# Optimization experiments

Measured on AMD Instinct MI355X. Metric: run time of the kernel, lower is better.

The kernel has to match this reference:

```python
import jax, jax.numpy as jnp
import numpy as np

DIM = 256  # channel width
B, H, W = 4, 64, 64


def conv2d(x, w, b, pad, groups=1):
    # x: NCHW, w: OIHW (I = C_in/groups)
    y = jax.lax.conv_general_dilated(
        x, w, window_strides=(1, 1),
        padding=[(pad[0], pad[0]), (pad[1], pad[1])],
        dimension_numbers=("NCHW", "OIHW", "NCHW"),
        feature_group_count=groups)
    return y + b[None, :, None, None]


def l2norm(x, eps=1e-12):
    # matches F.normalize(x, dim=-1): x / max(||x||_2, eps)
    n = jnp.sqrt(jnp.sum(x * x, axis=-1, keepdims=True))
    return x / jnp.maximum(n, eps)


def setup_inputs() -> dict:
    key = jax.random.key(0)
    ks = jax.random.split(key, 12)
    dim, c8 = DIM, DIM // 8
    w = lambda k, shape, s: jax.random.normal(k, shape, jnp.float32) * s
    return {
        "x": jax.random.normal(ks[0], (B, dim, H, W), jnp.float32),
        "w_conv": w(ks[1], (dim, dim, 3, 3), 0.02), "b_conv": jnp.zeros((dim,), jnp.float32),
        "w01": w(ks[2], (dim, 1, 1, 7), 0.05), "b01": jnp.zeros((dim,), jnp.float32),
        "w02": w(ks[3], (dim, 1, 7, 1), 0.05), "b02": jnp.zeros((dim,), jnp.float32),
        "w11": w(ks[4], (dim, 1, 1, 11), 0.05), "b11": jnp.zeros((dim,), jnp.float32),
        "w12": w(ks[5], (dim, 1, 11, 1), 0.05), "b12": jnp.zeros((dim,), jnp.float32),
        "w21": w(ks[6], (dim, 1, 1, 21), 0.05), "b21": jnp.zeros((dim,), jnp.float32),
        "w22": w(ks[7], (dim, 1, 21, 1), 0.05), "b22": jnp.zeros((dim,), jnp.float32),
        "w_proj": w(ks[8], (c8, dim, 1, 1), 0.05), "b_proj": jnp.zeros((c8,), jnp.float32),
        "w3": w(ks[9], (c8, dim // 4, 1, 1), 0.05), "b3": jnp.zeros((c8,), jnp.float32),
        "w4": w(ks[10], (dim, c8, 1, 1), 0.05), "b4": jnp.zeros((dim,), jnp.float32),
    }


def reference(x, w_conv, b_conv, w01, b01, w02, b02, w11, b11, w12, b12,
              w21, b21, w22, b22, w_proj, b_proj, w3, b3, w4, b4):
    b, c, h, w_ = x.shape
    x = conv2d(x, w_conv, b_conv, (1, 1))
    # multi-scale separable depthwise convs (7, 11, 21)
    x1 = conv2d(conv2d(x, w01, b01, (0, 3), c), w02, b02, (3, 0), c)
    x2 = conv2d(conv2d(x, w11, b11, (0, 5), c), w12, b12, (5, 0), c)
    x3 = conv2d(conv2d(x, w21, b21, (0, 10), c), w22, b22, (10, 0), c)
    out1 = x1 + x2 + x3 + x                      # [b, dim, h, w]
    out1 = conv2d(out1, w_proj, b_proj, (0, 0))  # [b, dim//8, h, w]
    c8 = out1.shape[1]
    t = out1.reshape(b, c8, h * w_)              # b head c (h w), head=1

    q1 = l2norm(t)
    attn1 = jax.nn.softmax(q1 @ jnp.swapaxes(q1, -2, -1), axis=-1)  # [b, c8, c8]
    out2 = attn1 @ t                                                # [b, c8, hw]

    # branch 2: spatial attention (hw x hw)
    ts = jnp.swapaxes(t, -2, -1)                 # [b, hw, c8]
    q2 = l2norm(ts)
    attn2 = jax.nn.softmax(q2 @ jnp.swapaxes(q2, -2, -1), axis=-1)  # [b, hw, hw]
    out3 = jnp.swapaxes(attn2 @ ts, -2, -1)                         # [b, c8, hw]

    out4 = jnp.concatenate([out2.reshape(b, c8, h, w_),
                            out3.reshape(b, c8, h, w_)], axis=1)    # [b, dim//4, h, w]
    out5 = conv2d(out4, w3, b3, (0, 0)) + out1
    return conv2d(out5, w4, b4, (0, 0))          # [b, dim, h, w]
```

## Files before the change

### kernel.cpp

```cpp
#include <hip/hip_runtime.h>
#include <hip/hip_bf16.h>

typedef __hip_bfloat16 bf16;
typedef short s16;
typedef __attribute__((ext_vector_type(4))) short s16x4;
typedef __attribute__((ext_vector_type(8))) short s16x8;
typedef __attribute__((ext_vector_type(4))) float f32x4;

__device__ __forceinline__ s16 f2b(float f){
    unsigned u = __float_as_uint(f);
    unsigned r = (u + 0x7FFFu + ((u >> 16) & 1u)) >> 16;
    return (s16)r;
}
__device__ __forceinline__ float b2f_bits(s16 v){
    return __uint_as_float(((unsigned)(unsigned short)v) << 16);
}

__global__ __launch_bounds__(256) void xtrans_k(const float* __restrict__ x, s16* __restrict__ xcl){
    __shared__ s16 lb[64][258];
    int h = blockIdx.x, b = blockIdx.y, t = threadIdx.x;
    for (int i = t; i < 16384; i += 256){
        int ci = i >> 6, w = i & 63;
        lb[w][ci] = f2b(x[((b*256 + ci)*64 + h)*64 + w]);
    }
    __syncthreads();
    for (int i = t; i < 16384; i += 256){
        int w = i >> 8, ci = i & 255;
        xcl[(b*4096 + h*64 + w)*256 + ci] = lb[w][ci];
    }
}

__global__ __launch_bounds__(256) void wpack_k(const float* __restrict__ w, s16* __restrict__ wpk){
    int idx = blockIdx.x*256 + threadIdx.x;
    int cil = idx & 31;
    int r   = idx >> 5;
    int co  = r & 255;
    int r2  = r >> 8;
    int tap = r2 % 9, cc = r2 / 9;
    wpk[idx] = f2b(w[(co*256 + cc*32 + cil)*9 + tap]);
}

__global__ __launch_bounds__(256) void conv3x3m_k(const s16* __restrict__ xcl,
        const s16* __restrict__ wpk, const float* __restrict__ bias,
        bf16* __restrict__ y0){
    __shared__ alignas(16) s16 smem[30240];
    s16* xls = smem;
    s16* wls = smem + 9504;
    const int sp = blockIdx.x, cog = blockIdx.y;
    const int b = sp >> 5, h0 = (sp & 31)*2;
    const int t = threadIdx.x;
    const int wv = t >> 6, lane = t & 63;
    const int lm = lane & 15, g = lane >> 4;

    f32x4 acc[2][4];
    #pragma unroll
    for (int mi = 0; mi < 2; ++mi)
        #pragma unroll
        for (int ni = 0; ni < 4; ++ni) acc[mi][ni] = (f32x4){0.f,0.f,0.f,0.f};

    for (int cc = 0; cc < 8; ++cc){
        __syncthreads();
        for (int i = t; i < 1056; i += 256){
            int g8 = i & 3, wi = (i>>2) % 66, r = (i>>2) / 66;
            int h = h0 - 1 + r, w = wi - 1;
            s16x8 v = {0,0,0,0,0,0,0,0};
            if (h >= 0 && h < 64 && w >= 0 && w < 64)
                v = *(const s16x8*)&xcl[(b*4096 + h*64 + w)*256 + cc*32 + g8*8];
            s16* d = &xls[(r*66 + wi)*36 + g8*8];
            *(s16x4*)d       = __builtin_shufflevector(v, v, 0,1,2,3);
            *(s16x4*)(d + 4) = __builtin_shufflevector(v, v, 4,5,6,7);
        }
        for (int i = t; i < 2304; i += 256){
            int g8 = i & 3, co = (i>>2) & 63, tap = i >> 8;
            s16x8 v = *(const s16x8*)&wpk[((cc*9 + tap)*256 + cog*64 + co)*32 + g8*8];
            s16* d = &wls[(tap*64 + co)*36 + g8*8];
            *(s16x4*)d       = __builtin_shufflevector(v, v, 0,1,2,3);
            *(s16x4*)(d + 4) = __builtin_shufflevector(v, v, 4,5,6,7);
        }
        __syncthreads();
        #pragma unroll
        for (int tap = 0; tap < 9; ++tap){
            const int kh = tap/3, kw = tap%3;
            s16x8 bfr[4], afr[2];
            #pragma unroll
            for (int ni = 0; ni < 4; ++ni){
                const s16* p = &wls[(tap*64 + ni*16 + lm)*36 + g*8];
                s16x4 lo = *(const s16x4*)p;
                s16x4 hi = *(const s16x4*)(p + 4);
                bfr[ni] = __builtin_shufflevector(lo, hi, 0,1,2,3,4,5,6,7);
            }
            #pragma unroll
            for (int mi = 0; mi < 2; ++mi){
                int m = (wv*2 + mi)*16 + lm;
                int hr = m >> 6, ww = m & 63;
                const s16* p = &xls[((hr + kh)*66 + (ww + kw))*36 + g*8];
                s16x4 lo = *(const s16x4*)p;
                s16x4 hi = *(const s16x4*)(p + 4);
                afr[mi] = __builtin_shufflevector(lo, hi, 0,1,2,3,4,5,6,7);
            }
            #pragma unroll
            for (int mi = 0; mi < 2; ++mi)
                #pragma unroll
                for (int ni = 0; ni < 4; ++ni)
                    acc[mi][ni] = __builtin_amdgcn_mfma_f32_16x16x32_bf16(
                        afr[mi], bfr[ni], acc[mi][ni], 0, 0, 0);
        }
    }
    __syncthreads();
    float* ot = (float*)smem;
    #pragma unroll
    for (int mi = 0; mi < 2; ++mi)
        #pragma unroll
        for (int ni = 0; ni < 4; ++ni)
            #pragma unroll
            for (int r = 0; r < 4; ++r){
                int m  = (wv*2 + mi)*16 + g*4 + r;
                int co = ni*16 + lm;
                ot[co*132 + m] = acc[mi][ni][r];
            }
    __syncthreads();
    for (int i = t; i < 8192; i += 256){
        int co = i >> 7, m = i & 127;
        float v = ot[co*132 + m] + bias[cog*64 + co];
        y0[((b*256 + cog*64 + co)*64 + h0 + (m>>6))*64 + (m & 63)] = __float2bfloat16(v);
    }
}

template<int K>
__device__ __forceinline__ void sep_branch(const float (*__restrict__ pl)[65], float (*__restrict__ hp)[65],
                                           int c, int t,
                                           const float* __restrict__ wh, const float* __restrict__ bh,
                                           const float* __restrict__ wv, const float* __restrict__ bv,
                                           float* acc){
    constexpr int P = K/2;
    constexpr int W = 16 + 2*P;
    float wk[K];
    #pragma unroll
    for (int j = 0; j < K; ++j) wk[j] = wh[c*K + j];
    float bhv = bh[c];
    {
        int h = t >> 2, w0 = (t & 3)*16;
        float win[W];
        #pragma unroll
        for (int j = 0; j < W; ++j){
            int ww = w0 - P + j;
            win[j] = (ww >= 0 && ww < 64) ? pl[h][ww] : 0.f;
        }
        __syncthreads();
        #pragma unroll
        for (int i = 0; i < 16; ++i){
            float s = bhv;
            #pragma unroll
            for (int k = 0; k < K; ++k) s += win[i+k]*wk[k];
            hp[h][w0 + i] = s;
        }
    }
    float vk[K];
    #pragma unroll
    for (int j = 0; j < K; ++j) vk[j] = wv[c*K + j];
    float bvv = bv[c];
    __syncthreads();
    {
        int w = t & 63, h0 = (t >> 6)*16;
        float win[W];
        #pragma unroll
        for (int j = 0; j < W; ++j){
            int hh = h0 - P + j;
            win[j] = (hh >= 0 && hh < 64) ? hp[hh][w] : 0.f;
        }
        #pragma unroll
        for (int i = 0; i < 16; ++i){
            float s = bvv;
            #pragma unroll
            for (int k = 0; k < K; ++k) s += win[i+k]*vk[k];
            acc[i] += s;
        }
    }
}

__global__ __launch_bounds__(256) void sepconv_k(const bf16* __restrict__ y0,
        const float* __restrict__ w01, const float* __restrict__ b01,
        const float* __restrict__ w02, const float* __restrict__ b02,
        const float* __restrict__ w11, const float* __restrict__ b11,
        const float* __restrict__ w12, const float* __restrict__ b12,
        const float* __restrict__ w21, const float* __restrict__ b21,
        const float* __restrict__ w22, const float* __restrict__ b22,
        bf16* __restrict__ out1){
    __shared__ float pl[64][65];
    __shared__ float hp[64][65];
    int bc = blockIdx.x;
    int c = bc & 255;
    int t = threadIdx.x;
    const bf16* src = y0 + bc*4096;
    for (int i = t; i < 4096; i += 256) pl[i>>6][i&63] = __bfloat162float(src[i]);
    __syncthreads();
    float acc[16];
    #pragma unroll
    for (int k = 0; k < 16; ++k) acc[k] = 0.f;
    sep_branch<7 >(pl, hp, c, t, w01, b01, w02, b02, acc);
    sep_branch<11>(pl, hp, c, t, w11, b11, w12, b12, acc);
    sep_branch<21>(pl, hp, c, t, w21, b21, w22, b22, acc);
    bf16* dst = out1 + bc*4096;
    {
        int w = t & 63, h0 = (t >> 6)*16;
        #pragma unroll
        for (int i = 0; i < 16; ++i)
            dst[(h0 + i)*64 + w] = __float2bfloat16(acc[i] + pl[h0 + i][w]);
    }
}

__global__ __launch_bounds__(256) void proj_k(const bf16* __restrict__ out1, const float* __restrict__ wp,
                                              const float* __restrict__ bp, float* __restrict__ tbuf,
                                              s16* __restrict__ tTb, float* __restrict__ rn2){
    __shared__ float wl[256*32];
    __shared__ s16 part[4][64][36];
    int pt = blockIdx.x, b = blockIdx.y, t = threadIdx.x;
    int q = t >> 6, lane = t & 63;
    for (int i = t; i < 8192; i += 256){
        int ci = i >> 5, cc = i & 31;
        wl[ci*32 + cc] = wp[cc*256 + ci];
    }
    __syncthreads();
    int p = pt*64 + lane;
    float acc[32] = {};
    const bf16* xb = out1 + b*1048576 + p;
    for (int ci = q*64; ci < q*64 + 64; ++ci){
        float v = __bfloat162float(xb[ci*4096]);
        const float* wr = &wl[ci*32];
        #pragma unroll
        for (int c8 = 0; c8 < 8; ++c8){
            float4 w4 = *(const float4*)&wr[c8*4];
            acc[c8*4+0] += w4.x*v; acc[c8*4+1] += w4.y*v;
            acc[c8*4+2] += w4.z*v; acc[c8*4+3] += w4.w*v;
        }
    }
    #pragma unroll
    for (int cc = 0; cc < 32; ++cc) part[q][lane][cc] = f2b(acc[cc]);
    __syncthreads();
    int p_loc = t >> 2, qq = t & 3;
    int pg = pt*64 + p_loc;
    float a8[8];
    float ss = 0.f;
    #pragma unroll
    for (int c = 0; c < 8; ++c){
        int cc = qq*8 + c;
        float v = b2f_bits(part[0][p_loc][cc]) + b2f_bits(part[1][p_loc][cc])
                + b2f_bits(part[2][p_loc][cc]) + b2f_bits(part[3][p_loc][cc]) + bp[cc];
        a8[c] = v;
        ss += v*v;
    }
    ss += __shfl_xor(ss, 1, 4);
    ss += __shfl_xor(ss, 2, 4);
    if (qq == 0) rn2[b*4096 + pg] = 1.f / fmaxf(sqrtf(ss), 1e-12f);
    #pragma unroll
    for (int c = 0; c < 8; ++c) tbuf[(b*32 + qq*8 + c)*4096 + pg] = a8[c];
    s16x8 o8;
    #pragma unroll
    for (int c = 0; c < 8; ++c) o8[c] = f2b(a8[c]);
    *(s16x8*)&tTb[(b*4096 + pg)*32 + qq*8] = o8;
}

__global__ __launch_bounds__(256) void gram2_k(const float* __restrict__ tbuf, float* __restrict__ part){
    __shared__ float tl[128][33];
    int ps = blockIdx.x, b = blockIdx.y, t = threadIdx.x;
    for (int idx = t; idx < 4096; idx += 256){
        int cc = idx >> 7, pp = idx & 127;
        tl[pp][cc] = tbuf[(b*32+cc)*4096 + ps*128 + pp];
    }
    __syncthreads();
    #pragma unroll
    for (int k = 0; k < 4; ++k){
        int pair = k*256 + t;
        int i = pair >> 5, j = pair & 31;
        float s = 0.f;
        #pragma unroll 4
        for (int pp = 0; pp < 128; ++pp) s += tl[pp][i]*tl[pp][j];
        part[(b*32+ps)*1024 + pair] = s;
    }
}

__global__ __launch_bounds__(64) void attn1_k(const float* __restrict__ part,
                                              float* __restrict__ attn1T){
    int i = blockIdx.x, b = blockIdx.y, j = threadIdx.x;
    float gij = 0.f, gjj = 0.f;
    if (j < 32){
        #pragma unroll 8
        for (int ps = 0; ps < 32; ++ps){
            const float* pp = part + (b*32+ps)*1024;
            gij += pp[i*32 + j];
            gjj += pp[j*33];
        }
    }
    float rnj = 1.f / fmaxf(sqrtf(gjj), 1e-12f);
    float rni = __shfl(rnj, i, 64);
    float e = (j < 32) ? __expf(rni*rnj*gij) : 0.f;
    float sum = e;
    #pragma unroll
    for (int o = 32; o > 0; o >>= 1) sum += __shfl_xor(sum, o, 64);
    if (j < 32) attn1T[b*1024 + j*32 + i] = e / sum;
}

__global__ __launch_bounds__(256) void fold_k(const float* __restrict__ attn1T,
        const float* __restrict__ w3, const float* __restrict__ b3,
        const float* __restrict__ w4, const float* __restrict__ b4,
        float* __restrict__ WtT, float* __restrict__ WoT, float* __restrict__ bfo){
    __shared__ float a1[1024];
    __shared__ float w3a[1024];
    __shared__ float w3bs[1024];
    int b = blockIdx.x, t = threadIdx.x;
    for (int idx = t; idx < 1024; idx += 256){
        int i = idx >> 5, j = idx & 31;
        a1[idx]   = attn1T[b*1024 + j*32 + i];
        w3bs[idx] = w3[i*64 + 32 + j];
    }
    __syncthreads();
    for (int idx = t; idx < 1024; idx += 256){
        int cc = idx >> 5, j = idx & 31;
        float s = 0.f;
        #pragma unroll 8
        for (int i = 0; i < 32; ++i) s += w3[cc*64 + i]*a1[i*32 + j];
        w3a[idx] = s;
    }
    __syncthreads();
    int co = t;
    float w4r[32];
    #pragma unroll
    for (int cc = 0; cc < 32; ++cc) w4r[cc] = w4[co*32 + cc];
    float bfv = b4[co];
    #pragma unroll
    for (int cc = 0; cc < 32; ++cc) bfv += w4r[cc]*b3[cc];
    bfo[b*256 + co] = bfv;
    for (int j = 0; j < 32; ++j){
        float st = w4r[j];
        float so = 0.f;
        #pragma unroll 8
        for (int cc = 0; cc < 32; ++cc){
            st += w4r[cc]*w3a[cc*32 + j];
            so += w4r[cc]*w3bs[cc*32 + j];
        }
        WtT[(b*32 + j)*256 + co] = st;
        WoT[(b*32 + j)*256 + co] = so;
    }
}

__global__ __launch_bounds__(256) void flashm_k(const s16* __restrict__ tTb, const float* __restrict__ rn2,
                                                float* __restrict__ partA, float* __restrict__ partL){
    __shared__ alignas(16) s16 kvb[128*36];
    __shared__ alignas(16) s16 vts[32*132];
    __shared__ alignas(16) s16 pls[4][16*132];
    __shared__ float rnj[128];
    __shared__ float ri[64];
    const int ib = blockIdx.x, b = blockIdx.y, chunk = blockIdx.z;
    const int t = threadIdx.x, wv = t >> 6, lane = t & 63;
    const int lm = lane & 15, g = lane >> 4;
    const int i0 = ib*64;

    if (t < 64) ri[t] = rn2[b*4096 + i0 + t];
    s16x8 qf = *(const s16x8*)&tTb[(b*4096 + i0 + wv*16 + lm)*32 + g*8];
    __syncthreads();
    float rni4[4];
    #pragma unroll
    for (int r = 0; r < 4; ++r) rni4[r] = ri[wv*16 + g*4 + r];

    f32x4 oacc[2];
    oacc[0] = (f32x4){0.f,0.f,0.f,0.f};
    oacc[1] = (f32x4){0.f,0.f,0.f,0.f};
    float lacc[4] = {0.f,0.f,0.f,0.f};
    s16* pw = pls[wv];

    for (int jt = chunk*16; jt < chunk*16 + 16; ++jt){
        const int j0 = jt*128;
        __syncthreads();
        for (int gi = t; gi < 512; gi += 256){
            int j = gi >> 2, g8 = gi & 3;
            s16x8 v = *(const s16x8*)&tTb[(b*4096 + j0 + j)*32 + g8*8];
            s16* d = &kvb[j*36 + g8*8];
            *(s16x4*)d       = __builtin_shufflevector(v, v, 0,1,2,3);
            *(s16x4*)(d + 4) = __builtin_shufflevector(v, v, 4,5,6,7);
            #pragma unroll
            for (int e = 0; e < 8; ++e) vts[(g8*8 + e)*132 + j] = v[e];
        }
        if (t < 128) rnj[t] = rn2[b*4096 + j0 + t];
        __syncthreads();
        #pragma unroll
        for (int nt = 0; nt < 8; ++nt){
            const s16* bp = &kvb[(nt*16 + lm)*36 + g*8];
            s16x4 blo = *(const s16x4*)bp;
            s16x4 bhi = *(const s16x4*)(bp + 4);
            s16x8 bf = __builtin_shufflevector(blo, bhi, 0,1,2,3,4,5,6,7);
            f32x4 s = __builtin_amdgcn_mfma_f32_16x16x32_bf16(qf, bf,
                        (f32x4){0.f,0.f,0.f,0.f}, 0, 0, 0);
            float rj = rnj[nt*16 + lm];
            #pragma unroll
            for (int r = 0; r < 4; ++r){
                float e = __expf(s[r]*rni4[r]*rj);
                lacc[r] += e;
                pw[(g*4 + r)*132 + nt*16 + lm] = f2b(e);
            }
        }
        #pragma unroll
        for (int ks = 0; ks < 4; ++ks){
            const s16* ap = &pw[lm*132 + ks*32 + g*8];
            s16x4 alo = *(const s16x4*)ap;
            s16x4 ahi = *(const s16x4*)(ap + 4);
            s16x8 af = __builtin_shufflevector(alo, ahi, 0,1,2,3,4,5,6,7);
            #pragma unroll
            for (int n2 = 0; n2 < 2; ++n2){
                const s16* vp = &vts[(n2*16 + lm)*132 + ks*32 + g*8];
                s16x4 vlo = *(const s16x4*)vp;
                s16x4 vhi = *(const s16x4*)(vp + 4);
                s16x8 vf = __builtin_shufflevector(vlo, vhi, 0,1,2,3,4,5,6,7);
                oacc[n2] = __builtin_amdgcn_mfma_f32_16x16x32_bf16(af, vf, oacc[n2], 0, 0, 0);
            }
        }
    }
    #pragma unroll
    for (int r = 0; r < 4; ++r){
        float v = lacc[r];
        v += __shfl_xor(v, 1, 16); v += __shfl_xor(v, 2, 16);
        v += __shfl_xor(v, 4, 16); v += __shfl_xor(v, 8, 16);
        lacc[r] = v;
    }
    const int base = (b*2 + chunk)*4096 + i0 + wv*16;
    #pragma unroll
    for (int n2 = 0; n2 < 2; ++n2)
        #pragma unroll
        for (int r = 0; r < 4; ++r)
            partA[(base + g*4 + r)*32 + n2*16 + lm] = oacc[n2][r];
    if (lm == 0){
        #pragma unroll
        for (int r = 0; r < 4; ++r) partL[base + g*4 + r] = lacc[r];
    }
}

__global__ __launch_bounds__(256) void finalfuse_k(const float* __restrict__ tbuf,
        const float* __restrict__ partA, const float* __restrict__ partL,
        const float* __restrict__ WtT, const float* __restrict__ WoT,
        const float* __restrict__ bfo, float* __restrict__ out){
    int pt = blockIdx.x, cog = blockIdx.y, b = blockIdx.z, t = threadIdx.x;
    int p = pt*256 + t;
    float l = partL[(b*2 + 0)*4096 + p] + partL[(b*2 + 1)*4096 + p];
    float inv = 1.f / l;
    const float* pa0 = partA + ((b*2 + 0)*4096 + p)*32;
    const float* pa1 = partA + ((b*2 + 1)*4096 + p)*32;
    float v3[32];
    #pragma unroll
    for (int q = 0; q < 8; ++q){
        float4 a = *(const float4*)&pa0[q*4];
        float4 c = *(const float4*)&pa1[q*4];
        v3[q*4+0] = (a.x + c.x)*inv; v3[q*4+1] = (a.y + c.y)*inv;
        v3[q*4+2] = (a.z + c.z)*inv; v3[q*4+3] = (a.w + c.w)*inv;
    }
    float acc[32];
    #pragma unroll
    for (int co = 0; co < 32; ++co) acc[co] = bfo[b*256 + cog*32 + co];
    for (int j = 0; j < 32; ++j){
        float vt = tbuf[(b*32 + j)*4096 + p];
        float vo = v3[j];
        const float* wtr = WtT + (b*32 + j)*256 + cog*32;
        const float* wor = WoT + (b*32 + j)*256 + cog*32;
        #pragma unroll
        for (int co = 0; co < 32; ++co) acc[co] += wtr[co]*vt + wor[co]*vo;
    }
    #pragma unroll
    for (int co = 0; co < 32; ++co)
        out[((b*256 + cog*32 + co)*4096) + p] = acc[co];
}

extern "C" void kernel_launch(void* const* d_in, const int* in_sizes, int n_in,
                              void* d_out, int out_size, void* d_ws, size_t ws_size,
                              hipStream_t stream) {
    const float* x      = (const float*)d_in[0];
    const float* w_conv = (const float*)d_in[1];
    const float* b_conv = (const float*)d_in[2];
    const float* w01 = (const float*)d_in[3];  const float* b01 = (const float*)d_in[4];
    const float* w02 = (const float*)d_in[5];  const float* b02 = (const float*)d_in[6];
    const float* w11 = (const float*)d_in[7];  const float* b11 = (const float*)d_in[8];
    const float* w12 = (const float*)d_in[9];  const float* b12 = (const float*)d_in[10];
    const float* w21 = (const float*)d_in[11]; const float* b21 = (const float*)d_in[12];
    const float* w22 = (const float*)d_in[13]; const float* b22 = (const float*)d_in[14];
    const float* w_proj = (const float*)d_in[15]; const float* b_proj = (const float*)d_in[16];
    const float* w3 = (const float*)d_in[17]; const float* b3 = (const float*)d_in[18];
    const float* w4 = (const float*)d_in[19]; const float* b4 = (const float*)d_in[20];

    char* wsb = (char*)d_ws;
    s16*   xcl  = (s16*)wsb;
    bf16*  out1 = (bf16*)wsb;
    bf16*  y0   = (bf16*)(wsb + 8388608);
    s16*   wpk  = (s16*)(wsb + 16777216);
    float* f    = (float*)d_ws;
    float* part   = f + 0;
    float* partA  = f + 0;
    float* tbuf   = f + 2097152;
    s16*   tTb    = (s16*)(wsb + 10485760);
    float* WtT    = f + 3145728;
    float* WoT    = f + 3178496;
    float* bfo    = f + 3211264;
    float* partL  = f + 4194304;
    float* attn1T = f + 4722816;
    float* rn2    = f + 4726912;

    xtrans_k<<<dim3(64, 4), 256, 0, stream>>>(x, xcl);
    wpack_k<<<dim3(2304), 256, 0, stream>>>(w_conv, wpk);
    conv3x3m_k<<<dim3(128, 4), 256, 0, stream>>>(xcl, wpk, b_conv, y0);
    sepconv_k<<<dim3(1024), 256, 0, stream>>>(y0, w01, b01, w02, b02,
                                              w11, b11, w12, b12,
                                              w21, b21, w22, b22, out1);
    proj_k<<<dim3(64, 4), 256, 0, stream>>>(out1, w_proj, b_proj, tbuf, tTb, rn2);
    gram2_k<<<dim3(32, 4), 256, 0, stream>>>(tbuf, part);
    attn1_k<<<dim3(32, 4), 64, 0, stream>>>(part, attn1T);
    fold_k<<<dim3(4), 256, 0, stream>>>(attn1T, w3, b3, w4, b4, WtT, WoT, bfo);
    flashm_k<<<dim3(64, 4, 2), 256, 0, stream>>>(tTb, rn2, partA, partL);
    finalfuse_k<<<dim3(16, 8, 4), 256, 0, stream>>>(tbuf, partA, partL, WtT, WoT, bfo,
                                                    (float*)d_out);
}
```

Baseline: 323.8 us.

## Shrink conv3x3 tile to one row and move channel Gram to MFMA

The 3x3 conv kernel now handles one output row per block instead of two, and stages weights three taps at a time. This cuts shared memory from about 60KB to 34KB so more blocks fit per CU, and it doubles the grid. The cost is more weight reloads and extra barriers per channel chunk. Separately, the 32x32 channel Gram matrix is now computed with bf16 MFMA over 256-pixel slices (16 partials) instead of scalar fp32 FMAs over 128-pixel slices, which lowers Gram precision to bf16 inputs.

```diff
diff --git a/kernel.cpp b/kernel.cpp
--- a/kernel.cpp
+++ b/kernel.cpp
@@ -43,24 +43,22 @@
 __global__ __launch_bounds__(256) void conv3x3m_k(const s16* __restrict__ xcl,
         const s16* __restrict__ wpk, const float* __restrict__ bias,
         bf16* __restrict__ y0){
-    __shared__ alignas(16) s16 smem[30240];
+    __shared__ alignas(16) s16 smem[16896];
     s16* xls = smem;
-    s16* wls = smem + 9504;
+    s16* wls = smem + 7128;
     const int sp = blockIdx.x, cog = blockIdx.y;
-    const int b = sp >> 5, h0 = (sp & 31)*2;
+    const int b = sp >> 6, h0 = sp & 63;
     const int t = threadIdx.x;
     const int wv = t >> 6, lane = t & 63;
     const int lm = lane & 15, g = lane >> 4;
 
-    f32x4 acc[2][4];
-    #pragma unroll
-    for (int mi = 0; mi < 2; ++mi)
-        #pragma unroll
-        for (int ni = 0; ni < 4; ++ni) acc[mi][ni] = (f32x4){0.f,0.f,0.f,0.f};
+    f32x4 acc[4];
+    #pragma unroll
+    for (int ni = 0; ni < 4; ++ni) acc[ni] = (f32x4){0.f,0.f,0.f,0.f};
 
     for (int cc = 0; cc < 8; ++cc){
         __syncthreads();
-        for (int i = t; i < 1056; i += 256){
+        for (int i = t; i < 792; i += 256){
             int g8 = i & 3, wi = (i>>2) % 66, r = (i>>2) / 66;
             int h = h0 - 1 + r, w = wi - 1;
             s16x8 v = {0,0,0,0,0,0,0,0};
@@ -70,59 +68,58 @@
             *(s16x4*)d       = __builtin_shufflevector(v, v, 0,1,2,3);
             *(s16x4*)(d + 4) = __builtin_shufflevector(v, v, 4,5,6,7);
         }
-        for (int i = t; i < 2304; i += 256){
-            int g8 = i & 3, co = (i>>2) & 63, tap = i >> 8;
-            s16x8 v = *(const s16x8*)&wpk[((cc*9 + tap)*256 + cog*64 + co)*32 + g8*8];
-            s16* d = &wls[(tap*64 + co)*36 + g8*8];
+        for (int i = t; i < 768; i += 256){
+            int g8 = i & 3, co = (i>>2) & 63, tl = i >> 8;
+            s16x8 v = *(const s16x8*)&wpk[((cc*9 + tl)*256 + cog*64 + co)*32 + g8*8];
+            s16* d = &wls[(tl*64 + co)*36 + g8*8];
             *(s16x4*)d       = __builtin_shufflevector(v, v, 0,1,2,3);
             *(s16x4*)(d + 4) = __builtin_shufflevector(v, v, 4,5,6,7);
         }
         __syncthreads();
-        #pragma unroll
-        for (int tap = 0; tap < 9; ++tap){
-            const int kh = tap/3, kw = tap%3;
-            s16x8 bfr[4], afr[2];
+        for (int tg = 0; tg < 3; ++tg){
             #pragma unroll
-            for (int ni = 0; ni < 4; ++ni){
-                const s16* p = &wls[(tap*64 + ni*16 + lm)*36 + g*8];
-                s16x4 lo = *(const s16x4*)p;
-                s16x4 hi = *(const s16x4*)(p + 4);
-                bfr[ni] = __builtin_shufflevector(lo, hi, 0,1,2,3,4,5,6,7);
+            for (int tl = 0; tl < 3; ++tl){
+                const s16* pa = &xls[(tg*66 + wv*16 + lm + tl)*36 + g*8];
+                s16x4 alo = *(const s16x4*)pa;
+                s16x4 ahi = *(const s16x4*)(pa + 4);
+                s16x8 af = __builtin_shufflevector(alo, ahi, 0,1,2,3,4,5,6,7);
+                #pragma unroll
+                for (int ni = 0; ni < 4; ++ni){
+                    const s16* pb = &wls[(tl*64 + ni*16 + lm)*36 + g*8];
+                    s16x4 blo = *(const s16x4*)pb;
+                    s16x4 bhi = *(const s16x4*)(pb + 4);
+                    s16x8 bf = __builtin_shufflevector(blo, bhi, 0,1,2,3,4,5,6,7);
+                    acc[ni] = __builtin_amdgcn_mfma_f32_16x16x32_bf16(af, bf, acc[ni], 0, 0, 0);
+                }
             }
-            #pragma unroll
-            for (int mi = 0; mi < 2; ++mi){
-                int m = (wv*2 + mi)*16 + lm;
-                int hr = m >> 6, ww = m & 63;
-                const s16* p = &xls[((hr + kh)*66 + (ww + kw))*36 + g*8];
-                s16x4 lo = *(const s16x4*)p;
-                s16x4 hi = *(const s16x4*)(p + 4);
-                afr[mi] = __builtin_shufflevector(lo, hi, 0,1,2,3,4,5,6,7);
+            if (tg < 2){
+                __syncthreads();
+                for (int i = t; i < 768; i += 256){
+                    int g8 = i & 3, co = (i>>2) & 63, tl = i >> 8;
+                    s16x8 v = *(const s16x8*)&wpk[((cc*9 + (tg+1)*3 + tl)*256 + cog*64 + co)*32 + g8*8];
+                    s16* d = &wls[(tl*64 + co)*36 + g8*8];
+                    *(s16x4*)d       = __builtin_shufflevector(v, v, 0,1,2,3);
+                    *(s16x4*)(d + 4) = __builtin_shufflevector(v, v, 4,5,6,7);
+                }
+                __syncthreads();
             }
-            #pragma unroll
-            for (int mi = 0; mi < 2; ++mi)
-                #pragma unroll
-                for (int ni = 0; ni < 4; ++ni)
-                    acc[mi][ni] = __builtin_amdgcn_mfma_f32_16x16x32_bf16(
-                        afr[mi], bfr[ni], acc[mi][ni], 0, 0, 0);
         }
     }
     __syncthreads();
     float* ot = (float*)smem;
     #pragma unroll
-    for (int mi = 0; mi < 2; ++mi)
-        #pragma unroll
-        for (int ni = 0; ni < 4; ++ni)
-            #pragma unroll
-            for (int r = 0; r < 4; ++r){
-                int m  = (wv*2 + mi)*16 + g*4 + r;
-                int co = ni*16 + lm;
-                ot[co*132 + m] = acc[mi][ni][r];
-            }
-    __syncthreads();
-    for (int i = t; i < 8192; i += 256){
-        int co = i >> 7, m = i & 127;
-        float v = ot[co*132 + m] + bias[cog*64 + co];
-        y0[((b*256 + cog*64 + co)*64 + h0 + (m>>6))*64 + (m & 63)] = __float2bfloat16(v);
+    for (int ni = 0; ni < 4; ++ni)
+        #pragma unroll
+        for (int r = 0; r < 4; ++r){
+            int m  = wv*16 + g*4 + r;
+            int co = ni*16 + lm;
+            ot[co*67 + m] = acc[ni][r];
+        }
+    __syncthreads();
+    for (int i = t; i < 4096; i += 256){
+        int co = i >> 6, m = i & 63;
+        float v = ot[co*67 + m] + bias[cog*64 + co];
+        y0[((b*256 + cog*64 + co)*64 + h0)*64 + m] = __float2bfloat16(v);
     }
 }
 
@@ -260,22 +257,47 @@
     *(s16x8*)&tTb[(b*4096 + pg)*32 + qq*8] = o8;
 }
 
-__global__ __launch_bounds__(256) void gram2_k(const float* __restrict__ tbuf, float* __restrict__ part){
-    __shared__ float tl[128][33];
-    int ps = blockIdx.x, b = blockIdx.y, t = threadIdx.x;
-    for (int idx = t; idx < 4096; idx += 256){
-        int cc = idx >> 7, pp = idx & 127;
-        tl[pp][cc] = tbuf[(b*32+cc)*4096 + ps*128 + pp];
-    }
-    __syncthreads();
-    #pragma unroll
-    for (int k = 0; k < 4; ++k){
-        int pair = k*256 + t;
-        int i = pair >> 5, j = pair & 31;
-        float s = 0.f;
-        #pragma unroll 4
-        for (int pp = 0; pp < 128; ++pp) s += tl[pp][i]*tl[pp][j];
-        part[(b*32+ps)*1024 + pair] = s;
+__global__ __launch_bounds__(256) void gramm_k(const float* __restrict__ tbuf, float* __restrict__ part){
+    __shared__ alignas(16) s16 ts[32*268];
+    int ks = blockIdx.x, b = blockIdx.y, t = threadIdx.x;
+    {
+        int cc = t >> 3, p0 = (t & 7)*32;
+        const float* src = tbuf + (b*32 + cc)*4096 + ks*256 + p0;
+        s16* d = &ts[cc*268 + p0];
+        #pragma unroll
+        for (int q = 0; q < 4; ++q){
+            float4 v0 = *(const float4*)&src[q*8];
+            float4 v1 = *(const float4*)&src[q*8 + 4];
+            s16x4 o0, o1;
+            o0[0]=f2b(v0.x); o0[1]=f2b(v0.y); o0[2]=f2b(v0.z); o0[3]=f2b(v0.w);
+            o1[0]=f2b(v1.x); o1[1]=f2b(v1.y); o1[2]=f2b(v1.z); o1[3]=f2b(v1.w);
+            *(s16x4*)&d[q*8]     = o0;
+            *(s16x4*)&d[q*8 + 4] = o1;
+        }
+    }
+    __syncthreads();
+    int wv = t >> 6, lane = t & 63, lm = lane & 15, g = lane >> 4;
+    int mi = wv >> 1, ni = wv & 1;
+    f32x4 acc = (f32x4){0.f,0.f,0.f,0.f};
+    const s16* ar = &ts[(mi*16 + lm)*268];
+    const s16* br = &ts[(ni*16 + lm)*268];
+    #pragma unroll
+    for (int kk = 0; kk < 8; ++kk){
+        const s16* ap = ar + kk*32 + g*8;
+        s16x4 alo = *(const s16x4*)ap;
+        s16x4 ahi = *(const s16x4*)(ap + 4);
+        s16x8 af = __builtin_shufflevector(alo, ahi, 0,1,2,3,4,5,6,7);
+        const s16* bp = br + kk*32 + g*8;
+        s16x4 blo = *(const s16x4*)bp;
+        s16x4 bhi = *(const s16x4*)(bp + 4);
+        s16x8 bf = __builtin_shufflevector(blo, bhi, 0,1,2,3,4,5,6,7);
+        acc = __builtin_amdgcn_mfma_f32_16x16x32_bf16(af, bf, acc, 0, 0, 0);
+    }
+    float* pd = part + (b*16 + ks)*1024;
+    #pragma unroll
+    for (int r = 0; r < 4; ++r){
+        int i = mi*16 + g*4 + r, j = ni*16 + lm;
+        pd[i*32 + j] = acc[r];
     }
 }
 
@@ -285,8 +307,8 @@
     float gij = 0.f, gjj = 0.f;
     if (j < 32){
         #pragma unroll 8
-        for (int ps = 0; ps < 32; ++ps){
-            const float* pp = part + (b*32+ps)*1024;
+        for (int ps = 0; ps < 16; ++ps){
+            const float* pp = part + (b*16+ps)*1024;
             gij += pp[i*32 + j];
             gjj += pp[j*33];
         }
@@ -502,12 +524,12 @@
 
     xtrans_k<<<dim3(64, 4), 256, 0, stream>>>(x, xcl);
     wpack_k<<<dim3(2304), 256, 0, stream>>>(w_conv, wpk);
-    conv3x3m_k<<<dim3(128, 4), 256, 0, stream>>>(xcl, wpk, b_conv, y0);
+    conv3x3m_k<<<dim3(256, 4), 256, 0, stream>>>(xcl, wpk, b_conv, y0);
     sepconv_k<<<dim3(1024), 256, 0, stream>>>(y0, w01, b01, w02, b02,
                                               w11, b11, w12, b12,
                                               w21, b21, w22, b22, out1);
     proj_k<<<dim3(64, 4), 256, 0, stream>>>(out1, w_proj, b_proj, tbuf, tTb, rn2);
-    gram2_k<<<dim3(32, 4), 256, 0, stream>>>(tbuf, part);
+    gramm_k<<<dim3(16, 4), 256, 0, stream>>>(tbuf, part);
     attn1_k<<<dim3(32, 4), 64, 0, stream>>>(part, attn1T);
     fold_k<<<dim3(4), 256, 0, stream>>>(attn1T, w3, b3, w4, b4, WtT, WoT, bfo);
     flashm_k<<<dim3(64, 4, 2), 256, 0, stream>>>(tTb, rn2, partA, partL);
```

Result: faster. 314.3 us (-2.9%).
